# Performance work log

Measured on AMD Instinct MI355X. Metric: run time of the kernel, lower is better.

Reference implementation:

```python
import math
import jax, jax.numpy as jnp
import numpy as np

N, T, F, H = 30000, 4, 128, 8  # num_node, num_type, num_fea, num_head
D = F // H


def setup_inputs() -> dict:
    key = jax.random.key(0)
    k0, k1, k2, k3, k4 = jax.random.split(key, 5)
    feature = jax.random.normal(k0, (N, F), dtype=jnp.float32)
    edge_fea = jax.random.normal(k1, (N, T, F), dtype=jnp.float32)
    node_multi_mask = jax.random.randint(k2, (N,), 0, T)
    # Xavier-uniform-like scale for [*, F, F] projection tables
    xav = math.sqrt(6.0 / (F + F))
    node_proj = jax.random.uniform(k3, (T, F, F), minval=-xav, maxval=xav, dtype=jnp.float32)
    edge_proj = jax.random.uniform(k4, (T * T, F, F), minval=-xav, maxval=xav, dtype=jnp.float32)
    return {
        "feature": feature,
        "edge_fea": edge_fea,
        "node_multi_mask": node_multi_mask,
        "node_proj": node_proj,
        "edge_proj": edge_proj,
    }


def reference(feature, edge_fea, node_multi_mask, node_proj, edge_proj):
    # Type-indexed projections. Instead of gathering per-node [F,F] matrices
    # (which would materialize N*F*F), compute projections for all T source
    # types in one batched einsum, then select each node's type with a gather.
    # node: out[n] = node_proj[mask[n]] @ feature[n]
    node_all = jnp.einsum('tgf,nf->ntg', node_proj, feature)           # [N,T,F]
    node_p = jnp.take_along_axis(node_all, node_multi_mask[:, None, None], axis=1)[:, 0]  # [N,F]
    # edge: out[n,j] = edge_proj[mask[n]*T + j] @ edge_fea[n,j]
    edge_proj_r = edge_proj.reshape(T, T, F, F)                         # [src_type, j, F, F]
    edge_all = jnp.einsum('stgf,ntf->nstg', edge_proj_r, edge_fea)      # [N,T_src,T,F]
    edge_p = jnp.take_along_axis(edge_all, node_multi_mask[:, None, None, None], axis=1)[:, 0]  # [N,T,F]

    # multi-head attention weights
    node_multi_in = node_p.reshape(N, 1, H, D).transpose(0, 2, 1, 3) / math.sqrt(D)  # [N,H,1,D]
    edge_multi_in = edge_p.reshape(N, T, H, D).transpose(0, 2, 3, 1)                  # [N,H,D,T]
    scores = jnp.matmul(node_multi_in, edge_multi_in)                                 # [N,H,1,T]
    # NOTE: original uses nn.Softmax(dim=1) -> softmax over the HEAD axis
    all_r_weight = jax.nn.softmax(scores, axis=1).transpose(0, 3, 1, 2)               # [N,T,H,1]
    return all_r_weight
```

## Files before the change

### kernel.cpp

```cpp
#include <hip/hip_runtime.h>
#include <hip/hip_bf16.h>

#define N_NODES 30000
#define T_TYPES 4
#define F_DIM   128
#define H_HEADS 8

typedef __bf16 bf16x8 __attribute__((ext_vector_type(8)));
typedef __bf16 bf16x4 __attribute__((ext_vector_type(4)));
typedef float  floatx4 __attribute__((ext_vector_type(4)));

#define WS_REORDER 64
#define WS_NPB     480256
#define WS_EPB     611328

__global__ __launch_bounds__(256) void prep_kernel(
    const float* __restrict__ node_proj, const float* __restrict__ edge_proj,
    __bf16* __restrict__ npb, __bf16* __restrict__ epb, int* __restrict__ counts)
{
    int i = blockIdx.x * 256 + threadIdx.x;
    if (i < 4) counts[i] = 0;
    int base = i * 4;
    float4 v;
    __bf16* dst;
    if (base < T_TYPES * F_DIM * F_DIM) {
        v = ((const float4*)node_proj)[i];
        dst = npb + base;
    } else {
        int off = base - T_TYPES * F_DIM * F_DIM;
        v = ((const float4*)edge_proj)[off >> 2];
        dst = epb + off;
    }
    bf16x4 w = { (__bf16)v.x, (__bf16)v.y, (__bf16)v.z, (__bf16)v.w };
    *(bf16x4*)dst = w;
}

__global__ __launch_bounds__(256) void bucket_kernel(
    const int* __restrict__ mask, int* __restrict__ counts, int* __restrict__ reorder)
{
    int n = blockIdx.x * 256 + threadIdx.x;
    int lane = threadIdx.x & 63;
    int t = (n < N_NODES) ? mask[n] : -1;
    #pragma unroll
    for (int tt = 0; tt < T_TYPES; ++tt) {
        unsigned long long b = __ballot(t == tt);
        if (b == 0ull) continue;
        int cnt = __popcll(b);
        int leader = __ffsll((unsigned long long)b) - 1;
        int base = 0;
        if (lane == leader) base = atomicAdd(&counts[tt], cnt);
        base = __shfl(base, leader);
        if (t == tt) {
            int prefix = __popcll(b & ((1ull << lane) - 1ull));
            reorder[tt * N_NODES + base + prefix] = n;
        }
    }
}

__global__ __launch_bounds__(256) void main_kernel(
    const float* __restrict__ feature, const float* __restrict__ edge_fea,
    const int* __restrict__ counts, const int* __restrict__ reorder,
    const __bf16* __restrict__ npb, const __bf16* __restrict__ epb,
    float* __restrict__ out)
{
    const int t = blockIdx.y;
    const int Nt = counts[t];
    const int start = blockIdx.x * 32;
    if (start >= Nt) return;
    const int valid = min(32, Nt - start);

    __shared__ __bf16 Afeat[32][136];
    __shared__ __bf16 Aedge[4][32][136];
    __shared__ float  sc[32][4][H_HEADS];
    __shared__ int    nidx[32];

    const int tid = threadIdx.x;
    if (tid < 32) {
        int s = (tid < valid) ? tid : (valid - 1);
        nidx[tid] = reorder[t * N_NODES + start + s];
    }
    __syncthreads();

    const int colv = tid & 31;
    const int rowg = tid >> 5;
    #pragma unroll
    for (int it = 0; it < 4; ++it) {
        int row = it * 8 + rowg;
        const float* src = feature + (long)nidx[row] * F_DIM;
        float4 v = ((const float4*)src)[colv];
        bf16x4 w = { (__bf16)v.x, (__bf16)v.y, (__bf16)v.z, (__bf16)v.w };
        *(bf16x4*)(&Afeat[row][0] + colv * 4) = w;
    }
    #pragma unroll
    for (int it = 0; it < 16; ++it) {
        int row = it * 8 + rowg;
        int j = row >> 5, r = row & 31;
        const float* src = edge_fea + ((long)nidx[r] * 4 + j) * F_DIM;
        float4 v = ((const float4*)src)[colv];
        bf16x4 w = { (__bf16)v.x, (__bf16)v.y, (__bf16)v.z, (__bf16)v.w };
        *(bf16x4*)(&Aedge[j][r][0] + colv * 4) = w;
    }
    __syncthreads();

    const int lane = tid & 63;
    const int wave = tid >> 6;
    const int ml   = lane & 15;
    const int quad = lane >> 4;
    const int g0   = wave * 32;

    floatx4 accN[2][2] = {};
    {
        const __bf16* a0 = &Afeat[ml][quad * 8];
        const __bf16* a1 = &Afeat[16 + ml][quad * 8];
        const __bf16* b0 = npb + t * (F_DIM * F_DIM) + (g0 + ml) * F_DIM + quad * 8;
        const __bf16* b1 = b0 + 16 * F_DIM;
        #pragma unroll
        for (int k0 = 0; k0 < 128; k0 += 32) {
            bf16x8 A0 = *(const bf16x8*)(a0 + k0);
            bf16x8 A1 = *(const bf16x8*)(a1 + k0);
            bf16x8 B0 = *(const bf16x8*)(b0 + k0);
            bf16x8 B1 = *(const bf16x8*)(b1 + k0);
            accN[0][0] = __builtin_amdgcn_mfma_f32_16x16x32_bf16(A0, B0, accN[0][0], 0, 0, 0);
            accN[0][1] = __builtin_amdgcn_mfma_f32_16x16x32_bf16(A0, B1, accN[0][1], 0, 0, 0);
            accN[1][0] = __builtin_amdgcn_mfma_f32_16x16x32_bf16(A1, B0, accN[1][0], 0, 0, 0);
            accN[1][1] = __builtin_amdgcn_mfma_f32_16x16x32_bf16(A1, B1, accN[1][1], 0, 0, 0);
        }
    }

    #pragma unroll
    for (int j = 0; j < 4; ++j) {
        floatx4 accE[2][2] = {};
        const __bf16* a0 = &Aedge[j][ml][quad * 8];
        const __bf16* a1 = &Aedge[j][16 + ml][quad * 8];
        const __bf16* b0 = epb + (t * 4 + j) * (F_DIM * F_DIM) + (g0 + ml) * F_DIM + quad * 8;
        const __bf16* b1 = b0 + 16 * F_DIM;
        #pragma unroll
        for (int k0 = 0; k0 < 128; k0 += 32) {
            bf16x8 A0 = *(const bf16x8*)(a0 + k0);
            bf16x8 A1 = *(const bf16x8*)(a1 + k0);
            bf16x8 B0 = *(const bf16x8*)(b0 + k0);
            bf16x8 B1 = *(const bf16x8*)(b1 + k0);
            accE[0][0] = __builtin_amdgcn_mfma_f32_16x16x32_bf16(A0, B0, accE[0][0], 0, 0, 0);
            accE[0][1] = __builtin_amdgcn_mfma_f32_16x16x32_bf16(A0, B1, accE[0][1], 0, 0, 0);
            accE[1][0] = __builtin_amdgcn_mfma_f32_16x16x32_bf16(A1, B0, accE[1][0], 0, 0, 0);
            accE[1][1] = __builtin_amdgcn_mfma_f32_16x16x32_bf16(A1, B1, accE[1][1], 0, 0, 0);
        }
        #pragma unroll
        for (int mt = 0; mt < 2; ++mt) {
            #pragma unroll
            for (int nt = 0; nt < 2; ++nt) {
                floatx4 p = accN[mt][nt] * accE[mt][nt];
                #pragma unroll
                for (int s = 1; s < 16; s <<= 1) {
                    p.x += __shfl_xor(p.x, s);
                    p.y += __shfl_xor(p.y, s);
                    p.z += __shfl_xor(p.z, s);
                    p.w += __shfl_xor(p.w, s);
                }
                if (ml == 0) {
                    int h = wave * 2 + nt;
                    int mb = mt * 16 + quad * 4;
                    sc[mb + 0][j][h] = p.x * 0.25f;
                    sc[mb + 1][j][h] = p.y * 0.25f;
                    sc[mb + 2][j][h] = p.z * 0.25f;
                    sc[mb + 3][j][h] = p.w * 0.25f;
                }
            }
        }
    }
    __syncthreads();

    if (tid < 128) {
        int node = tid >> 2, j = tid & 3;
        if (node < valid) {
            float v[8], m = -1e30f;
            #pragma unroll
            for (int h = 0; h < 8; ++h) { v[h] = sc[node][j][h]; m = fmaxf(m, v[h]); }
            float s = 0.f;
            #pragma unroll
            for (int h = 0; h < 8; ++h) { v[h] = __expf(v[h] - m); s += v[h]; }
            float r = 1.0f / s;
            float* o = out + (long)nidx[node] * (T_TYPES * H_HEADS) + j * H_HEADS;
            float4 o0 = { v[0] * r, v[1] * r, v[2] * r, v[3] * r };
            float4 o1 = { v[4] * r, v[5] * r, v[6] * r, v[7] * r };
            ((float4*)o)[0] = o0;
            ((float4*)o)[1] = o1;
        }
    }
}

extern "C" void kernel_launch(void* const* d_in, const int* in_sizes, int n_in,
                              void* d_out, int out_size, void* d_ws, size_t ws_size,
                              hipStream_t stream) {
    const float* feature   = (const float*)d_in[0];
    const float* edge_fea  = (const float*)d_in[1];
    const int*   mask      = (const int*)d_in[2];
    const float* node_proj = (const float*)d_in[3];
    const float* edge_proj = (const float*)d_in[4];
    float* out = (float*)d_out;

    char* ws = (char*)d_ws;
    int*    counts  = (int*)ws;
    int*    reorder = (int*)(ws + WS_REORDER);
    __bf16* npb     = (__bf16*)(ws + WS_NPB);
    __bf16* epb     = (__bf16*)(ws + WS_EPB);

    prep_kernel<<<320, 256, 0, stream>>>(node_proj, edge_proj, npb, epb, counts);
    bucket_kernel<<<(N_NODES + 255) / 256, 256, 0, stream>>>(mask, counts, reorder);
    dim3 grid((N_NODES + 31) / 32, T_TYPES);
    main_kernel<<<grid, 256, 0, stream>>>(feature, edge_fea, counts, reorder, npb, epb, out);
}
```

Baseline: 158.7 us.

## Split heads across eight waves, use DPP row reductions, interleave type blocks

The main kernel now runs 512 threads per block, so each of the 8 waves computes a single head's 16 output columns instead of two heads per wave. The 16-lane score reductions switch from __shfl_xor chains to DPP quad_perm and row-mirror adds, which avoids LDS-permute traffic. The 2D grid is flattened so consecutive blocks cycle through node types, spreading the early-exiting blocks of sparsely populated types across the launch. In exchange, each wave issues fewer MFMAs and has less independent work to hide latency, and the larger blocks may change occupancy.

```diff
diff --git a/kernel.cpp b/kernel.cpp
--- a/kernel.cpp
+++ b/kernel.cpp
@@ -13,6 +13,20 @@
 #define WS_REORDER 64
 #define WS_NPB     480256
 #define WS_EPB     611328
+
+template <int CTRL>
+static __device__ __forceinline__ float dpp_add(float x) {
+    int xi = __builtin_bit_cast(int, x);
+    int yi = __builtin_amdgcn_update_dpp(xi, xi, CTRL, 0xF, 0xF, true);
+    return x + __builtin_bit_cast(float, yi);
+}
+static __device__ __forceinline__ float sum16(float x) {
+    x = dpp_add<0xB1>(x);
+    x = dpp_add<0x4E>(x);
+    x = dpp_add<0x141>(x);
+    x = dpp_add<0x140>(x);
+    return x;
+}
 
 __global__ __launch_bounds__(256) void prep_kernel(
     const float* __restrict__ node_proj, const float* __restrict__ edge_proj,
@@ -57,15 +71,16 @@
     }
 }
 
-__global__ __launch_bounds__(256) void main_kernel(
+__global__ __launch_bounds__(512) void main_kernel(
     const float* __restrict__ feature, const float* __restrict__ edge_fea,
     const int* __restrict__ counts, const int* __restrict__ reorder,
     const __bf16* __restrict__ npb, const __bf16* __restrict__ epb,
     float* __restrict__ out)
 {
-    const int t = blockIdx.y;
+    const int b = blockIdx.x;
+    const int t = b & 3;
+    const int start = (b >> 2) * 32;
     const int Nt = counts[t];
-    const int start = blockIdx.x * 32;
     if (start >= Nt) return;
     const int valid = min(32, Nt - start);
 
@@ -84,19 +99,17 @@
     const int colv = tid & 31;
     const int rowg = tid >> 5;
     #pragma unroll
-    for (int it = 0; it < 4; ++it) {
-        int row = it * 8 + rowg;
-        const float* src = feature + (long)nidx[row] * F_DIM;
-        float4 v = ((const float4*)src)[colv];
+    for (int it = 0; it < 2; ++it) {
+        int row = it * 16 + rowg;
+        float4 v = ((const float4*)(feature + (long)nidx[row] * F_DIM))[colv];
         bf16x4 w = { (__bf16)v.x, (__bf16)v.y, (__bf16)v.z, (__bf16)v.w };
         *(bf16x4*)(&Afeat[row][0] + colv * 4) = w;
     }
     #pragma unroll
-    for (int it = 0; it < 16; ++it) {
-        int row = it * 8 + rowg;
+    for (int it = 0; it < 8; ++it) {
+        int row = it * 16 + rowg;
         int j = row >> 5, r = row & 31;
-        const float* src = edge_fea + ((long)nidx[r] * 4 + j) * F_DIM;
-        float4 v = ((const float4*)src)[colv];
+        float4 v = ((const float4*)(edge_fea + ((long)nidx[r] * 4 + j) * F_DIM))[colv];
         bf16x4 w = { (__bf16)v.x, (__bf16)v.y, (__bf16)v.z, (__bf16)v.w };
         *(bf16x4*)(&Aedge[j][r][0] + colv * 4) = w;
     }
@@ -106,65 +119,50 @@
     const int wave = tid >> 6;
     const int ml   = lane & 15;
     const int quad = lane >> 4;
-    const int g0   = wave * 32;
-
-    floatx4 accN[2][2] = {};
+    const int g0   = wave * 16;
+
+    floatx4 accN[2] = {};
     {
         const __bf16* a0 = &Afeat[ml][quad * 8];
         const __bf16* a1 = &Afeat[16 + ml][quad * 8];
         const __bf16* b0 = npb + t * (F_DIM * F_DIM) + (g0 + ml) * F_DIM + quad * 8;
-        const __bf16* b1 = b0 + 16 * F_DIM;
         #pragma unroll
         for (int k0 = 0; k0 < 128; k0 += 32) {
             bf16x8 A0 = *(const bf16x8*)(a0 + k0);
             bf16x8 A1 = *(const bf16x8*)(a1 + k0);
             bf16x8 B0 = *(const bf16x8*)(b0 + k0);
-            bf16x8 B1 = *(const bf16x8*)(b1 + k0);
-            accN[0][0] = __builtin_amdgcn_mfma_f32_16x16x32_bf16(A0, B0, accN[0][0], 0, 0, 0);
-            accN[0][1] = __builtin_amdgcn_mfma_f32_16x16x32_bf16(A0, B1, accN[0][1], 0, 0, 0);
-            accN[1][0] = __builtin_amdgcn_mfma_f32_16x16x32_bf16(A1, B0, accN[1][0], 0, 0, 0);
-            accN[1][1] = __builtin_amdgcn_mfma_f32_16x16x32_bf16(A1, B1, accN[1][1], 0, 0, 0);
+            accN[0] = __builtin_amdgcn_mfma_f32_16x16x32_bf16(A0, B0, accN[0], 0, 0, 0);
+            accN[1] = __builtin_amdgcn_mfma_f32_16x16x32_bf16(A1, B0, accN[1], 0, 0, 0);
         }
     }
 
     #pragma unroll
     for (int j = 0; j < 4; ++j) {
-        floatx4 accE[2][2] = {};
+        floatx4 accE[2] = {};
         const __bf16* a0 = &Aedge[j][ml][quad * 8];
         const __bf16* a1 = &Aedge[j][16 + ml][quad * 8];
         const __bf16* b0 = epb + (t * 4 + j) * (F_DIM * F_DIM) + (g0 + ml) * F_DIM + quad * 8;
-        const __bf16* b1 = b0 + 16 * F_DIM;
         #pragma unroll
         for (int k0 = 0; k0 < 128; k0 += 32) {
             bf16x8 A0 = *(const bf16x8*)(a0 + k0);
             bf16x8 A1 = *(const bf16x8*)(a1 + k0);
             bf16x8 B0 = *(const bf16x8*)(b0 + k0);
-            bf16x8 B1 = *(const bf16x8*)(b1 + k0);
-            accE[0][0] = __builtin_amdgcn_mfma_f32_16x16x32_bf16(A0, B0, accE[0][0], 0, 0, 0);
-            accE[0][1] = __builtin_amdgcn_mfma_f32_16x16x32_bf16(A0, B1, accE[0][1], 0, 0, 0);
-            accE[1][0] = __builtin_amdgcn_mfma_f32_16x16x32_bf16(A1, B0, accE[1][0], 0, 0, 0);
-            accE[1][1] = __builtin_amdgcn_mfma_f32_16x16x32_bf16(A1, B1, accE[1][1], 0, 0, 0);
+            accE[0] = __builtin_amdgcn_mfma_f32_16x16x32_bf16(A0, B0, accE[0], 0, 0, 0);
+            accE[1] = __builtin_amdgcn_mfma_f32_16x16x32_bf16(A1, B0, accE[1], 0, 0, 0);
         }
         #pragma unroll
         for (int mt = 0; mt < 2; ++mt) {
-            #pragma unroll
-            for (int nt = 0; nt < 2; ++nt) {
-                floatx4 p = accN[mt][nt] * accE[mt][nt];
-                #pragma unroll
-                for (int s = 1; s < 16; s <<= 1) {
-                    p.x += __shfl_xor(p.x, s);
-                    p.y += __shfl_xor(p.y, s);
-                    p.z += __shfl_xor(p.z, s);
-                    p.w += __shfl_xor(p.w, s);
-                }
-                if (ml == 0) {
-                    int h = wave * 2 + nt;
-                    int mb = mt * 16 + quad * 4;
-                    sc[mb + 0][j][h] = p.x * 0.25f;
-                    sc[mb + 1][j][h] = p.y * 0.25f;
-                    sc[mb + 2][j][h] = p.z * 0.25f;
-                    sc[mb + 3][j][h] = p.w * 0.25f;
-                }
+            floatx4 p = accN[mt] * accE[mt];
+            p.x = sum16(p.x);
+            p.y = sum16(p.y);
+            p.z = sum16(p.z);
+            p.w = sum16(p.w);
+            if (ml == 0) {
+                int mb = mt * 16 + quad * 4;
+                sc[mb + 0][j][wave] = p.x * 0.25f;
+                sc[mb + 1][j][wave] = p.y * 0.25f;
+                sc[mb + 2][j][wave] = p.z * 0.25f;
+                sc[mb + 3][j][wave] = p.w * 0.25f;
             }
         }
     }
@@ -207,6 +205,6 @@
 
     prep_kernel<<<320, 256, 0, stream>>>(node_proj, edge_proj, npb, epb, counts);
     bucket_kernel<<<(N_NODES + 255) / 256, 256, 0, stream>>>(mask, counts, reorder);
-    dim3 grid((N_NODES + 31) / 32, T_TYPES);
-    main_kernel<<<grid, 256, 0, stream>>>(feature, edge_fea, counts, reorder, npb, epb, out);
-}
+    int nblk = ((N_NODES + 31) / 32) * T_TYPES;
+    main_kernel<<<nblk, 512, 0, stream>>>(feature, edge_fea, counts, reorder, npb, epb, out);
+}
```

After: 144.9 us. 1.09x faster.
